# Kernel tuning notes

Hardware: AMD Instinct MI355X
Metric: run time of the kernel (lower is better)

## Reference

```python
import jax, jax.numpy as jnp
import numpy as np

EPS = 1e-10
B, S, D, K = 8, 2048, 512, 1024
TEMP = 1.0  # quantizer temperature set to 1.0 in SQVAE.__init__


def _ln(x, g, b):
    m = x.mean(-1, keepdims=True)
    v = x.var(-1, keepdims=True)
    return (x - m) / jnp.sqrt(v + 1e-5) * g + b


def _mlp(x, w1, b1, g1, be1, w2, b2, g2, be2):
    # feed_forward: Linear -> ReLU -> LayerNorm, twice (MLPLayers=2)
    h = _ln(jax.nn.relu(x @ w1 + b1), g1, be1)
    return _ln(jax.nn.relu(h @ w2 + b2), g2, be2)


def setup_inputs() -> dict:
    key = jax.random.key(0)
    ks = jax.random.split(key, 20)
    W = 0.04  # small init scale to keep distances / softmax well-conditioned
    p = lambda k, sh, s=1.0: jax.random.normal(k, sh, dtype=jnp.float32) * s
    return {
        'x': p(ks[0], (B, S, D)),
        'gumbel_u': jax.random.uniform(ks[1], (B * S, K), dtype=jnp.float32),
        'enc_w1': p(ks[2], (D, D), W), 'enc_b1': jnp.zeros(D, jnp.float32),
        'enc_g1': jnp.ones(D, jnp.float32), 'enc_be1': jnp.zeros(D, jnp.float32),
        'enc_w2': p(ks[3], (D, D), W), 'enc_b2': jnp.zeros(D, jnp.float32),
        'enc_g2': jnp.ones(D, jnp.float32), 'enc_be2': jnp.zeros(D, jnp.float32),
        'dec_w1': p(ks[4], (D, D), W), 'dec_b1': jnp.zeros(D, jnp.float32),
        'dec_g1': jnp.ones(D, jnp.float32), 'dec_be1': jnp.zeros(D, jnp.float32),
        'dec_w2': p(ks[5], (D, D), W), 'dec_b2': jnp.zeros(D, jnp.float32),
        'dec_g2': jnp.ones(D, jnp.float32), 'dec_be2': jnp.zeros(D, jnp.float32),
        'codebook': p(ks[6], (K, D)),
        'log_param_q': jnp.zeros((), jnp.float32),
    }


def reference(x, gumbel_u, enc_w1, enc_b1, enc_g1, enc_be1, enc_w2, enc_b2, enc_g2, enc_be2,
              dec_w1, dec_b1, dec_g1, dec_be1, dec_w2, dec_b2, dec_g2, dec_be2,
              codebook, log_param_q):
    bs, seq, d = x.shape
    z = _mlp(x, enc_w1, enc_b1, enc_g1, enc_be1, enc_w2, enc_b2, enc_g2, enc_be2)
    # gaussian_1: log_var_q = 0 -> var_q = exp(log_param_q_scalar)
    var_q = jnp.exp(log_param_q)
    w = 0.5 / jnp.clip(var_q, 1e-10)  # 0.5 * precision_q (scalar)
    zf = z.reshape(-1, d)  # [N, D]
    # cdist^2 style distance, scaled by weight -> logits [N, K]
    dist = w * (jnp.sum(zf * zf, axis=1, keepdims=True)
                + jnp.sum(codebook * codebook, axis=1)
                - 2.0 * zf @ codebook.T)
    logit = -dist
    logp = jax.nn.log_softmax(logit, axis=-1)
    probs = jnp.exp(logp)
    # gumbel-softmax sample (train path), noise provided as uniform input
    g = -jnp.log(-jnp.log(gumbel_u + EPS) + EPS)
    encodings = jax.nn.softmax((logit + g) / TEMP, axis=-1)
    z_q = (encodings @ codebook).reshape(bs, seq, d)
    kld_discrete = jnp.sum(probs * logp) / bs
    kld_continuous = jnp.mean(jnp.sum((z - z_q) ** 2 * w, axis=(1, 2)))
    loss = kld_discrete + kld_continuous
    avg_probs = jnp.mean(jax.lax.stop_gradient(probs), axis=0)
    perplexity = jnp.exp(-jnp.sum(avg_probs * jnp.log(avg_probs + 1e-7)))
    x_rec = _mlp(z_q, dec_w1, dec_b1, dec_g1, dec_be1, dec_w2, dec_b2, dec_g2, dec_be2)
    return x_rec, loss, perplexity
```

## Files before the change

### kernel.cpp

```cpp
#include <hip/hip_runtime.h>
#include <math.h>

#define NROWS 16384
#define DIM   512
#define KCODE 1024

typedef __attribute__((ext_vector_type(8))) __bf16 bf16x8;
typedef __attribute__((ext_vector_type(4))) float f32x4;

__device__ __forceinline__ float wave_reduce_sum(float v) {
  #pragma unroll
  for (int m = 1; m < 64; m <<= 1) v += __shfl_xor(v, m, 64);
  return v;
}
__device__ __forceinline__ float wave_reduce_max(float v) {
  #pragma unroll
  for (int m = 1; m < 64; m <<= 1) v = fmaxf(v, __shfl_xor(v, m, 64));
  return v;
}
__device__ __forceinline__ unsigned short f2bf(float f) {
  union { float f; unsigned u; } v; v.f = f;
  unsigned r = v.u + 0x7FFFu + ((v.u >> 16) & 1u);
  return (unsigned short)(r >> 16);
}
__device__ __forceinline__ float bf2f(unsigned short h) {
  union { unsigned u; float f; } v; v.u = ((unsigned)h) << 16;
  return v.f;
}
__device__ __forceinline__ uint4 pack8(const float* x) {
  uint4 r;
  r.x = (unsigned)f2bf(x[0]) | ((unsigned)f2bf(x[1]) << 16);
  r.y = (unsigned)f2bf(x[2]) | ((unsigned)f2bf(x[3]) << 16);
  r.z = (unsigned)f2bf(x[4]) | ((unsigned)f2bf(x[5]) << 16);
  r.w = (unsigned)f2bf(x[6]) | ((unsigned)f2bf(x[7]) << 16);
  return r;
}

__device__ __forceinline__ void glds16(const void* g, void* lds) {
  __builtin_amdgcn_global_load_lds(
      (const __attribute__((address_space(1))) unsigned int*)g,
      (__attribute__((address_space(3))) unsigned int*)lds, 16, 0, 0);
}

__global__ __launch_bounds__(512, 2) void dist_fused(
    const unsigned short* __restrict__ zhp, const unsigned short* __restrict__ zlp,
    const unsigned short* __restrict__ cbh, const unsigned short* __restrict__ cbl,
    const float* __restrict__ znorm, const float* __restrict__ cnorm,
    const float* __restrict__ lpq, float* __restrict__ outf) {
  __shared__ char smem[131072];
  const int t = threadIdx.x;
  const int l = t & 63, w = t >> 6;
  const int wm = w >> 2, wn = w & 3;
  const int b = blockIdx.x;
  const int xcd = b & 7, j = b >> 3;
  const int m0 = (xcd * 8 + j / 4) * 256;
  const int n0 = (j % 4) * 256;

  f32x4 acc[8][4];
  #pragma unroll
  for (int i = 0; i < 8; ++i)
    #pragma unroll
    for (int jj = 0; jj < 4; ++jj) acc[i][jj] = (f32x4){0.f, 0.f, 0.f, 0.f};

  const int row = l & 15;
  const int kcol = (l >> 4) * 8;
  const size_t aLo = (size_t)(m0 + w * 16 + row) * 512 + kcol;
  const size_t aHi = aLo + (size_t)128 * 512;
  const size_t bLo = (size_t)(n0 + w * 16 + row) * 512 + kcol;
  const size_t bHi = bLo + (size_t)128 * 512;
  const int dLo = w * 2048, dHi = (w + 8) * 2048;

  #pragma unroll 1
  for (int s = 0; s < 8; ++s) {
    const int kt = s * 64;
    #pragma unroll
    for (int js = 0; js < 2; ++js) {
      const int ko = kt + js * 32;
      const int dj = js * 1024;
      glds16(zhp + aLo + ko, smem + dLo + dj);
      glds16(zhp + aHi + ko, smem + dHi + dj);
      glds16(zlp + aLo + ko, smem + 32768 + dLo + dj);
      glds16(zlp + aHi + ko, smem + 32768 + dHi + dj);
      glds16(cbh + bLo + ko, smem + 65536 + dLo + dj);
      glds16(cbh + bHi + ko, smem + 65536 + dHi + dj);
      glds16(cbl + bLo + ko, smem + 98304 + dLo + dj);
      glds16(cbl + bHi + ko, smem + 98304 + dHi + dj);
    }
    asm volatile("s_waitcnt vmcnt(0)" ::: "memory");
    __builtin_amdgcn_s_barrier();
    #pragma unroll
    for (int js = 0; js < 2; ++js) {
      const int dj = js * 1024;
      bf16x8 af[8], bh_[4], bl_[4];
      #pragma unroll
      for (int i = 0; i < 4; ++i) {
        bh_[i] = *(const bf16x8*)(smem + 65536 + (wn * 4 + i) * 2048 + dj + l * 16);
        bl_[i] = *(const bf16x8*)(smem + 98304 + (wn * 4 + i) * 2048 + dj + l * 16);
      }
      #pragma unroll
      for (int i = 0; i < 8; ++i)
        af[i] = *(const bf16x8*)(smem + (wm * 8 + i) * 2048 + dj + l * 16);
      #pragma unroll
      for (int mi = 0; mi < 8; ++mi)
        #pragma unroll
        for (int ni = 0; ni < 4; ++ni) {
          acc[mi][ni] = __builtin_amdgcn_mfma_f32_16x16x32_bf16(af[mi], bh_[ni], acc[mi][ni], 0, 0, 0);
          acc[mi][ni] = __builtin_amdgcn_mfma_f32_16x16x32_bf16(af[mi], bl_[ni], acc[mi][ni], 0, 0, 0);
        }
      #pragma unroll
      for (int i = 0; i < 8; ++i)
        af[i] = *(const bf16x8*)(smem + 32768 + (wm * 8 + i) * 2048 + dj + l * 16);
      #pragma unroll
      for (int mi = 0; mi < 8; ++mi)
        #pragma unroll
        for (int ni = 0; ni < 4; ++ni)
          acc[mi][ni] = __builtin_amdgcn_mfma_f32_16x16x32_bf16(af[mi], bh_[ni], acc[mi][ni], 0, 0, 0);
    }
    __builtin_amdgcn_s_barrier();
  }

  float* slab = (float*)(smem + w * 4352);
  const int q = l >> 4, c16 = l & 15;
  const int c4 = (l & 15) * 4;
  const float wq = 0.5f / fmaxf(expf(lpq[0]), 1e-10f);

  #pragma unroll
  for (int mi = 0; mi < 8; ++mi) {
    __syncthreads();
    #pragma unroll
    for (int ni = 0; ni < 4; ++ni)
      #pragma unroll
      for (int r = 0; r < 4; ++r)
        slab[(q * 4 + r) * 68 + ni * 16 + c16] = acc[mi][ni][r];
    __syncthreads();
    #pragma unroll
    for (int pp = 0; pp < 4; ++pp) {
      const int rw = pp * 4 + q;
      const float4 v4 = *(const float4*)&slab[rw * 68 + c4];
      const int m = m0 + wm * 128 + mi * 16 + rw;
      const int nc = n0 + wn * 64 + c4;
      const float zn = znorm[m];
      const float4 cn = *(const float4*)&cnorm[nc];
      float4 o;
      o.x = -wq * (zn + cn.x - 2.f * v4.x);
      o.y = -wq * (zn + cn.y - 2.f * v4.y);
      o.z = -wq * (zn + cn.z - 2.f * v4.z);
      o.w = -wq * (zn + cn.w - 2.f * v4.w);
      *(float4*)&outf[(size_t)m * KCODE + nc] = o;
    }
  }
}

template <int EPI, int K, int N, int LDA>
__global__ __launch_bounds__(256) void gemm_bt(
    const unsigned short* A0, const unsigned short* B0,
    const float* __restrict__ bias, const float* __restrict__ lpq,
    const unsigned short* __restrict__ zh, const unsigned short* __restrict__ zl,
    float* __restrict__ kldc, unsigned short* __restrict__ outb) {
  __shared__ char smem[65536];
  const int t = threadIdx.x;
  const int l = t & 63, w = t >> 6;
  const int wm = w >> 1, wn = w & 1;
  const int NTN = N / 128;
  const int b = blockIdx.x;
  const int xcd = b & 7;
  const int j = b >> 3;
  const int m0 = (xcd * 16 + j / NTN) * 128;
  const int n0 = (j % NTN) * 128;

  f32x4 acc[4][4];
  #pragma unroll
  for (int i = 0; i < 4; ++i)
    #pragma unroll
    for (int jj = 0; jj < 4; ++jj) acc[i][jj] = (f32x4){0.f, 0.f, 0.f, 0.f};

  const int row = l & 15;
  const int kcol = (l >> 4) * 8;
  const size_t oA0 = (size_t)(m0 + w * 16 + row) * LDA + kcol;
  const size_t oA1 = oA0 + (size_t)64 * LDA;
  const size_t oB0 = (size_t)(n0 + w * 16 + row) * K + kcol;
  const size_t oB1 = oB0 + (size_t)64 * K;
  const int dLo = w * 2048, dHi = (w + 4) * 2048;

  constexpr int NSTEP = K / 64;

  auto issue = [&](int ss) {
    char* hb = smem + (ss & 1) * 32768;
    const int kt = ss * 64;
    #pragma unroll
    for (int js = 0; js < 2; ++js) {
      const int ko = kt + js * 32;
      const int dj = js * 1024;
      glds16(A0 + oA0 + ko, hb + dLo + dj);
      glds16(A0 + oA1 + ko, hb + dHi + dj);
      glds16(B0 + oB0 + ko, hb + 16384 + dLo + dj);
      glds16(B0 + oB1 + ko, hb + 16384 + dHi + dj);
    }
  };

  issue(0);
  #pragma unroll 1
  for (int s = 0; s < NSTEP; ++s) {
    if (s + 1 < NSTEP) {
      issue(s + 1);
      asm volatile("s_waitcnt vmcnt(8)" ::: "memory");
    } else {
      asm volatile("s_waitcnt vmcnt(0)" ::: "memory");
    }
    __builtin_amdgcn_s_barrier();
    const char* hb = smem + (s & 1) * 32768;
    #pragma unroll
    for (int js = 0; js < 2; ++js) {
      const int dj = js * 1024;
      bf16x8 af[4], bfr[4];
      #pragma unroll
      for (int i = 0; i < 4; ++i) {
        af[i]  = *(const bf16x8*)(hb + (wm * 4 + i) * 2048 + dj + l * 16);
        bfr[i] = *(const bf16x8*)(hb + 16384 + (wn * 4 + i) * 2048 + dj + l * 16);
      }
      #pragma unroll
      for (int mi = 0; mi < 4; ++mi)
        #pragma unroll
        for (int ni = 0; ni < 4; ++ni)
          acc[mi][ni] = __builtin_amdgcn_mfma_f32_16x16x32_bf16(af[mi], bfr[ni], acc[mi][ni], 0, 0, 0);
    }
    __builtin_amdgcn_s_barrier();
  }

  float* slab = (float*)(smem + w * 4352);
  const int q = l >> 4, c16 = l & 15;
  const int c4 = (l & 15) * 4;
  const float wq = (EPI == 2) ? 0.5f / fmaxf(expf(lpq[0]), 1e-10f) : 0.f;
  float local = 0.f;

  #pragma unroll
  for (int mi = 0; mi < 4; ++mi) {
    __syncthreads();
    #pragma unroll
    for (int ni = 0; ni < 4; ++ni)
      #pragma unroll
      for (int r = 0; r < 4; ++r)
        slab[(q * 4 + r) * 68 + ni * 16 + c16] = acc[mi][ni][r];
    __syncthreads();
    #pragma unroll
    for (int pp = 0; pp < 4; ++pp) {
      const int rw = pp * 4 + q;
      const float4 v4 = *(const float4*)&slab[rw * 68 + c4];
      float v[4] = {v4.x, v4.y, v4.z, v4.w};
      const int m = m0 + wm * 64 + mi * 16 + rw;
      const int nc = n0 + wn * 64 + c4;
      if (EPI == 0) {
        const float4 b4 = *(const float4*)&bias[nc];
        v[0] = fmaxf(v[0] + b4.x, 0.f);
        v[1] = fmaxf(v[1] + b4.y, 0.f);
        v[2] = fmaxf(v[2] + b4.z, 0.f);
        v[3] = fmaxf(v[3] + b4.w, 0.f);
        uint2 st;
        st.x = (unsigned)f2bf(v[0]) | ((unsigned)f2bf(v[1]) << 16);
        st.y = (unsigned)f2bf(v[2]) | ((unsigned)f2bf(v[3]) << 16);
        *(uint2*)&outb[(size_t)m * N + nc] = st;
      } else {
        const uint2 h2 = *(const uint2*)&zh[(size_t)m * N + nc];
        const uint2 l2 = *(const uint2*)&zl[(size_t)m * N + nc];
        const float z0 = bf2f((unsigned short)(h2.x & 0xFFFF)) + bf2f((unsigned short)(l2.x & 0xFFFF));
        const float z1 = bf2f((unsigned short)(h2.x >> 16))    + bf2f((unsigned short)(l2.x >> 16));
        const float z2 = bf2f((unsigned short)(h2.y & 0xFFFF)) + bf2f((unsigned short)(l2.y & 0xFFFF));
        const float z3 = bf2f((unsigned short)(h2.y >> 16))    + bf2f((unsigned short)(l2.y >> 16));
        const float d0 = z0 - v[0], d1 = z1 - v[1], d2 = z2 - v[2], d3 = z3 - v[3];
        local += d0 * d0 + d1 * d1 + d2 * d2 + d3 * d3;
        uint2 st;
        st.x = (unsigned)f2bf(v[0]) | ((unsigned)f2bf(v[1]) << 16);
        st.y = (unsigned)f2bf(v[2]) | ((unsigned)f2bf(v[3]) << 16);
        *(uint2*)&outb[(size_t)m * N + nc] = st;
      }
    }
  }
  if (EPI == 2) {
    local = wave_reduce_sum(local) * wq;
    if (l == 0) atomicAdd(kldc, local);
  }
}

template <int MODE>
__global__ __launch_bounds__(256) void ln_rows(
    const unsigned short* __restrict__ X, const float* __restrict__ g,
    const float* __restrict__ be, unsigned short* __restrict__ Y,
    unsigned short* __restrict__ Yl, float* __restrict__ znorm,
    float* __restrict__ Yf) {
  const int l = threadIdx.x & 63, wv = threadIdx.x >> 6;
  float gv[8], bv[8];
  {
    const float4 a = *(const float4*)&g[l * 8];
    const float4 b = *(const float4*)&g[l * 8 + 4];
    gv[0] = a.x; gv[1] = a.y; gv[2] = a.z; gv[3] = a.w;
    gv[4] = b.x; gv[5] = b.y; gv[6] = b.z; gv[7] = b.w;
    const float4 c = *(const float4*)&be[l * 8];
    const float4 d = *(const float4*)&be[l * 8 + 4];
    bv[0] = c.x; bv[1] = c.y; bv[2] = c.z; bv[3] = c.w;
    bv[4] = d.x; bv[5] = d.y; bv[6] = d.z; bv[7] = d.w;
  }
  const int row0 = blockIdx.x * 32 + wv * 8;
  for (int rr = 0; rr < 8; ++rr) {
    const int row = row0 + rr;
    const uint4 raw = *(const uint4*)&X[(size_t)row * 512 + l * 8];
    float v[8];
    const unsigned rw[4] = {raw.x, raw.y, raw.z, raw.w};
    #pragma unroll
    for (int i = 0; i < 4; ++i) {
      v[2 * i]     = bf2f((unsigned short)(rw[i] & 0xFFFF));
      v[2 * i + 1] = bf2f((unsigned short)(rw[i] >> 16));
    }
    float s = 0.f, ss = 0.f;
    #pragma unroll
    for (int i = 0; i < 8; ++i) { s += v[i]; ss += v[i] * v[i]; }
    #pragma unroll
    for (int m = 1; m < 64; m <<= 1) {
      s += __shfl_xor(s, m, 64);
      ss += __shfl_xor(ss, m, 64);
    }
    const float mean = s * (1.f / 512.f);
    const float var = ss * (1.f / 512.f) - mean * mean;
    const float rstd = rsqrtf(var + 1e-5f);
    float y[8];
    #pragma unroll
    for (int i = 0; i < 8; ++i) y[i] = (v[i] - mean) * rstd * gv[i] + bv[i];
    if (MODE == 0) {
      *(uint4*)&Y[(size_t)row * 512 + l * 8] = pack8(y);
    } else if (MODE == 1) {
      float lo[8], ns = 0.f;
      unsigned short hx[8];
      #pragma unroll
      for (int i = 0; i < 8; ++i) {
        hx[i] = f2bf(y[i]);
        lo[i] = y[i] - bf2f(hx[i]);
        ns += y[i] * y[i];
      }
      uint4 hv;
      hv.x = (unsigned)hx[0] | ((unsigned)hx[1] << 16);
      hv.y = (unsigned)hx[2] | ((unsigned)hx[3] << 16);
      hv.z = (unsigned)hx[4] | ((unsigned)hx[5] << 16);
      hv.w = (unsigned)hx[6] | ((unsigned)hx[7] << 16);
      *(uint4*)&Y[(size_t)row * 512 + l * 8] = hv;
      *(uint4*)&Yl[(size_t)row * 512 + l * 8] = pack8(lo);
      ns = wave_reduce_sum(ns);
      if (l == 0) znorm[row] = ns;
    } else {
      float4 o0, o1;
      o0.x = y[0]; o0.y = y[1]; o0.z = y[2]; o0.w = y[3];
      o1.x = y[4]; o1.y = y[5]; o1.z = y[6]; o1.w = y[7];
      *(float4*)&Yf[(size_t)row * 512 + l * 8] = o0;
      *(float4*)&Yf[(size_t)row * 512 + l * 8 + 4] = o1;
    }
  }
}

__global__ __launch_bounds__(256) void convert_f32_bf16(
    const float* __restrict__ X, unsigned short* __restrict__ Y) {
  const size_t i = ((size_t)blockIdx.x * 256 + threadIdx.x) * 8;
  const float4 a = *(const float4*)&X[i];
  const float4 b = *(const float4*)&X[i + 4];
  float v[8] = {a.x, a.y, a.z, a.w, b.x, b.y, b.z, b.w};
  *(uint4*)&Y[i] = pack8(v);
}

__global__ __launch_bounds__(256) void prep_cb(
    const float* __restrict__ CB, unsigned short* __restrict__ H,
    unsigned short* __restrict__ L, float* __restrict__ cnorm) {
  const int wv = threadIdx.x >> 6, l = threadIdx.x & 63;
  const int r = blockIdx.x * 4 + wv;
  const float* row = &CB[(size_t)r * 512 + l * 8];
  const float4 a = *(const float4*)row;
  const float4 b = *(const float4*)(row + 4);
  float x[8] = {a.x, a.y, a.z, a.w, b.x, b.y, b.z, b.w};
  float s = 0.f, lo[8];
  unsigned short hi[8];
  #pragma unroll
  for (int i = 0; i < 8; ++i) {
    s += x[i] * x[i];
    hi[i] = f2bf(x[i]);
    lo[i] = x[i] - bf2f(hi[i]);
  }
  uint4 hv;
  hv.x = (unsigned)hi[0] | ((unsigned)hi[1] << 16);
  hv.y = (unsigned)hi[2] | ((unsigned)hi[3] << 16);
  hv.z = (unsigned)hi[4] | ((unsigned)hi[5] << 16);
  hv.w = (unsigned)hi[6] | ((unsigned)hi[7] << 16);
  *(uint4*)&H[(size_t)r * 512 + l * 8] = hv;
  *(uint4*)&L[(size_t)r * 512 + l * 8] = pack8(lo);
  s = wave_reduce_sum(s);
  if (l == 0) cnorm[r] = s;
}

__global__ __launch_bounds__(256) void transpose_f32_bf16(
    const float* __restrict__ in, unsigned short* __restrict__ out, int R, int C) {
  __shared__ float tile[32][33];
  const int ntc = C >> 5;
  const int c0 = (blockIdx.x % ntc) * 32, r0 = (blockIdx.x / ntc) * 32;
  const int tx = threadIdx.x & 31, ty = threadIdx.x >> 5;
  #pragma unroll
  for (int i = 0; i < 4; ++i)
    tile[ty + 8 * i][tx] = in[(size_t)(r0 + ty + 8 * i) * C + c0 + tx];
  __syncthreads();
  #pragma unroll
  for (int i = 0; i < 4; ++i)
    out[(size_t)(c0 + ty + 8 * i) * R + r0 + tx] = f2bf(tile[tx][ty + 8 * i]);
}

__global__ __launch_bounds__(256) void softmax_gumbel(
    const float* logits, const float* __restrict__ U, unsigned short* E,
    float* __restrict__ colsum, float* __restrict__ kldd_acc) {
  __shared__ float cs[1024];
  __shared__ float kd[4];
  const int t = threadIdx.x;
  const int wv = t >> 6, l = t & 63;
  #pragma unroll
  for (int i = 0; i < 4; ++i) cs[t + 256 * i] = 0.f;
  __syncthreads();
  float psum[16];
  #pragma unroll
  for (int i = 0; i < 16; ++i) psum[i] = 0.f;
  float kldd = 0.f;
  const int nbase = blockIdx.x * 16 + wv * 4;

  for (int it = 0; it < 4; ++it) {
    const int row = nbase + it;
    const size_t off = (size_t)row * KCODE + 4 * l;
    float v[16];
    #pragma unroll
    for (int jj = 0; jj < 4; ++jj) {
      const float4 t4 = *(const float4*)&logits[off + 256 * jj];
      v[4 * jj + 0] = t4.x; v[4 * jj + 1] = t4.y; v[4 * jj + 2] = t4.z; v[4 * jj + 3] = t4.w;
    }
    float m = v[0];
    #pragma unroll
    for (int i = 1; i < 16; ++i) m = fmaxf(m, v[i]);
    m = wave_reduce_max(m);
    float e[16], se = 0.f;
    #pragma unroll
    for (int i = 0; i < 16; ++i) { e[i] = __expf(v[i] - m); se += e[i]; }
    se = wave_reduce_sum(se);
    const float lz = __logf(se);
    const float inv_se = 1.f / se;
    float pl = 0.f;
    #pragma unroll
    for (int i = 0; i < 16; ++i) {
      const float p = e[i] * inv_se;
      psum[i] += p;
      pl += p * (v[i] - m - lz);
    }
    kldd += pl;
    float y[16];
    #pragma unroll
    for (int jj = 0; jj < 4; ++jj) {
      const float4 t4 = *(const float4*)&U[off + 256 * jj];
      y[4 * jj + 0] = v[4 * jj + 0] - __logf(-__logf(t4.x + 1e-10f) + 1e-10f);
      y[4 * jj + 1] = v[4 * jj + 1] - __logf(-__logf(t4.y + 1e-10f) + 1e-10f);
      y[4 * jj + 2] = v[4 * jj + 2] - __logf(-__logf(t4.z + 1e-10f) + 1e-10f);
      y[4 * jj + 3] = v[4 * jj + 3] - __logf(-__logf(t4.w + 1e-10f) + 1e-10f);
    }
    float m2 = y[0];
    #pragma unroll
    for (int i = 1; i < 16; ++i) m2 = fmaxf(m2, y[i]);
    m2 = wave_reduce_max(m2);
    float ey[16], s2 = 0.f;
    #pragma unroll
    for (int i = 0; i < 16; ++i) { ey[i] = __expf(y[i] - m2); s2 += ey[i]; }
    s2 = wave_reduce_sum(s2);
    const float inv = 1.f / s2;
    #pragma unroll
    for (int jj = 0; jj < 4; ++jj) {
      ushort4 e4;
      e4.x = f2bf(ey[4 * jj + 0] * inv);
      e4.y = f2bf(ey[4 * jj + 1] * inv);
      e4.z = f2bf(ey[4 * jj + 2] * inv);
      e4.w = f2bf(ey[4 * jj + 3] * inv);
      *(ushort4*)&E[(size_t)row * 2048 + 4 * l + 256 * jj] = e4;
    }
  }
  #pragma unroll
  for (int jj = 0; jj < 4; ++jj)
    #pragma unroll
    for (int c = 0; c < 4; ++c)
      atomicAdd(&cs[256 * jj + 4 * l + c], psum[4 * jj + c]);
  kldd = wave_reduce_sum(kldd);
  if (l == 0) kd[wv] = kldd;
  __syncthreads();
  #pragma unroll
  for (int i = 0; i < 4; ++i) {
    const float vv = cs[t + 256 * i];
    if (vv != 0.f) atomicAdd(&colsum[t + 256 * i], vv);
  }
  if (t == 0) atomicAdd(kldd_acc, kd[0] + kd[1] + kd[2] + kd[3]);
}

__global__ __launch_bounds__(256) void finalize(
    const float* __restrict__ colsum, const float* __restrict__ scal,
    float* __restrict__ out) {
  const int t = threadIdx.x;
  float ent = 0.f;
  #pragma unroll
  for (int jj = 0; jj < 4; ++jj) {
    const float a = colsum[t + 256 * jj] * (1.f / 16384.f);
    ent += a * logf(a + 1e-7f);
  }
  ent = wave_reduce_sum(ent);
  __shared__ float red[4];
  if ((t & 63) == 0) red[t >> 6] = ent;
  __syncthreads();
  if (t == 0) {
    const float tot = red[0] + red[1] + red[2] + red[3];
    out[0] = (scal[0] + scal[1]) * (1.f / 8.f);
    out[1] = expf(-tot);
  }
}

extern "C" void kernel_launch(void* const* d_in, const int* in_sizes, int n_in,
                              void* d_out, int out_size, void* d_ws, size_t ws_size,
                              hipStream_t stream) {
  const float* x      = (const float*)d_in[0];
  const float* gu     = (const float*)d_in[1];
  const float* enc_w1 = (const float*)d_in[2];
  const float* enc_b1 = (const float*)d_in[3];
  const float* enc_g1 = (const float*)d_in[4];
  const float* enc_e1 = (const float*)d_in[5];
  const float* enc_w2 = (const float*)d_in[6];
  const float* enc_b2 = (const float*)d_in[7];
  const float* enc_g2 = (const float*)d_in[8];
  const float* enc_e2 = (const float*)d_in[9];
  const float* dec_w1 = (const float*)d_in[10];
  const float* dec_b1 = (const float*)d_in[11];
  const float* dec_g1 = (const float*)d_in[12];
  const float* dec_e1 = (const float*)d_in[13];
  const float* dec_w2 = (const float*)d_in[14];
  const float* dec_b2 = (const float*)d_in[15];
  const float* dec_g2 = (const float*)d_in[16];
  const float* dec_e2 = (const float*)d_in[17];
  const float* cb     = (const float*)d_in[18];
  const float* lpq    = (const float*)d_in[19];
  float* out = (float*)d_out;
  char* wsb = (char*)d_ws;

  float*          logits = (float*)(wsb + 0);
  unsigned short* Eb     = (unsigned short*)(wsb + 0);
  unsigned short* t1     = (unsigned short*)(wsb + 67108864);
  unsigned short* xb     = (unsigned short*)(wsb + 83886080);
  unsigned short* zh     = xb;
  unsigned short* hq     = (unsigned short*)(wsb + 100663296);
  unsigned short* zl     = (unsigned short*)(wsb + 117440512);
  unsigned short* wt0    = (unsigned short*)(wsb + 134217728);
  unsigned short* wt1    = wt0 + 262144;
  unsigned short* wt2    = wt1 + 262144;
  unsigned short* wt3    = wt2 + 262144;
  unsigned short* cbh    = (unsigned short*)(wsb + 136314880);
  unsigned short* cbl    = (unsigned short*)(wsb + 137363456);
  unsigned short* cbT    = (unsigned short*)(wsb + 138412032);
  float*          znorm  = (float*)(wsb + 139460608);
  float*          cnorm  = (float*)(wsb + 139526144);
  float*          colsum = (float*)(wsb + 139530240);
  float*          scal   = (float*)(wsb + 139534336);

  hipMemsetAsync(colsum, 0, 4096 + 16, stream);

  convert_f32_bf16<<<4096, 256, 0, stream>>>(x, xb);
  prep_cb<<<256, 256, 0, stream>>>(cb, cbh, cbl, cnorm);
  transpose_f32_bf16<<<256, 256, 0, stream>>>(enc_w1, wt0, 512, 512);
  transpose_f32_bf16<<<256, 256, 0, stream>>>(enc_w2, wt1, 512, 512);
  transpose_f32_bf16<<<256, 256, 0, stream>>>(dec_w1, wt2, 512, 512);
  transpose_f32_bf16<<<256, 256, 0, stream>>>(dec_w2, wt3, 512, 512);
  transpose_f32_bf16<<<512, 256, 0, stream>>>(cb, cbT, 1024, 512);

  gemm_bt<0, 512, 512, 512><<<512, 256, 0, stream>>>(
      xb, wt0, enc_b1, nullptr, nullptr, nullptr, nullptr, t1);
  ln_rows<0><<<512, 256, 0, stream>>>(t1, enc_g1, enc_e1, hq, nullptr, nullptr, nullptr);
  gemm_bt<0, 512, 512, 512><<<512, 256, 0, stream>>>(
      hq, wt1, enc_b2, nullptr, nullptr, nullptr, nullptr, t1);
  ln_rows<1><<<512, 256, 0, stream>>>(t1, enc_g2, enc_e2, zh, zl, znorm, nullptr);
  dist_fused<<<256, 512, 0, stream>>>(
      zh, zl, cbh, cbl, znorm, cnorm, lpq, logits);
  softmax_gumbel<<<1024, 256, 0, stream>>>(logits, gu, Eb, colsum, &scal[0]);
  gemm_bt<2, 1024, 512, 2048><<<512, 256, 0, stream>>>(
      Eb, cbT, nullptr, lpq, zh, zl, &scal[1], hq);
  gemm_bt<0, 512, 512, 512><<<512, 256, 0, stream>>>(
      hq, wt2, dec_b1, nullptr, nullptr, nullptr, nullptr, t1);
  ln_rows<0><<<512, 256, 0, stream>>>(t1, dec_g1, dec_e1, zl, nullptr, nullptr, nullptr);
  gemm_bt<0, 512, 512, 512><<<512, 256, 0, stream>>>(
      zl, wt3, dec_b2, nullptr, nullptr, nullptr, nullptr, t1);
  ln_rows<2><<<512, 256, 0, stream>>>(t1, dec_g2, dec_e2, nullptr, nullptr, nullptr, out);
  finalize<<<1, 256, 0, stream>>>(colsum, scal, out + 8388608);
}
```

Measured before the change: 469.9 us.

## Shrink dist_fused tiles to 128x128 and double-buffer LDS loads

```diff
diff --git a/kernel.cpp b/kernel.cpp
--- a/kernel.cpp
+++ b/kernel.cpp
@@ -42,80 +42,82 @@
       (__attribute__((address_space(3))) unsigned int*)lds, 16, 0, 0);
 }
 
-__global__ __launch_bounds__(512, 2) void dist_fused(
+__global__ __launch_bounds__(256) void dist_fused(
     const unsigned short* __restrict__ zhp, const unsigned short* __restrict__ zlp,
     const unsigned short* __restrict__ cbh, const unsigned short* __restrict__ cbl,
     const float* __restrict__ znorm, const float* __restrict__ cnorm,
     const float* __restrict__ lpq, float* __restrict__ outf) {
-  __shared__ char smem[131072];
+  __shared__ char smem[65536];
   const int t = threadIdx.x;
   const int l = t & 63, w = t >> 6;
-  const int wm = w >> 2, wn = w & 3;
+  const int wm = w >> 1, wn = w & 1;
   const int b = blockIdx.x;
   const int xcd = b & 7, j = b >> 3;
-  const int m0 = (xcd * 8 + j / 4) * 256;
-  const int n0 = (j % 4) * 256;
-
-  f32x4 acc[8][4];
-  #pragma unroll
-  for (int i = 0; i < 8; ++i)
+  const int m0 = (xcd * 16 + j / 8) * 128;
+  const int n0 = (j % 8) * 128;
+
+  f32x4 acc[4][4];
+  #pragma unroll
+  for (int i = 0; i < 4; ++i)
     #pragma unroll
     for (int jj = 0; jj < 4; ++jj) acc[i][jj] = (f32x4){0.f, 0.f, 0.f, 0.f};
 
   const int row = l & 15;
   const int kcol = (l >> 4) * 8;
   const size_t aLo = (size_t)(m0 + w * 16 + row) * 512 + kcol;
-  const size_t aHi = aLo + (size_t)128 * 512;
+  const size_t aHi = aLo + (size_t)64 * 512;
   const size_t bLo = (size_t)(n0 + w * 16 + row) * 512 + kcol;
-  const size_t bHi = bLo + (size_t)128 * 512;
-  const int dLo = w * 2048, dHi = (w + 8) * 2048;
-
+  const size_t bHi = bLo + (size_t)64 * 512;
+  const int dLo = w * 1024, dHi = (w + 4) * 1024;
+
+  auto issue = [&](int s) {
+    char* hb = smem + (s & 1) * 32768;
+    const int kt = s * 32;
+    glds16(zhp + aLo + kt, hb + dLo);
+    glds16(zhp + aHi + kt, hb + dHi);
+    glds16(zlp + aLo + kt, hb + 8192 + dLo);
+    glds16(zlp + aHi + kt, hb + 8192 + dHi);
+    glds16(cbh + bLo + kt, hb + 16384 + dLo);
+    glds16(cbh + bHi + kt, hb + 16384 + dHi);
+    glds16(cbl + bLo + kt, hb + 24576 + dLo);
+    glds16(cbl + bHi + kt, hb + 24576 + dHi);
+  };
+
+  issue(0);
   #pragma unroll 1
-  for (int s = 0; s < 8; ++s) {
-    const int kt = s * 64;
-    #pragma unroll
-    for (int js = 0; js < 2; ++js) {
-      const int ko = kt + js * 32;
-      const int dj = js * 1024;
-      glds16(zhp + aLo + ko, smem + dLo + dj);
-      glds16(zhp + aHi + ko, smem + dHi + dj);
-      glds16(zlp + aLo + ko, smem + 32768 + dLo + dj);
-      glds16(zlp + aHi + ko, smem + 32768 + dHi + dj);
-      glds16(cbh + bLo + ko, smem + 65536 + dLo + dj);
-      glds16(cbh + bHi + ko, smem + 65536 + dHi + dj);
-      glds16(cbl + bLo + ko, smem + 98304 + dLo + dj);
-      glds16(cbl + bHi + ko, smem + 98304 + dHi + dj);
-    }
-    asm volatile("s_waitcnt vmcnt(0)" ::: "memory");
+  for (int s = 0; s < 16; ++s) {
+    if (s + 1 < 16) {
+      issue(s + 1);
+      asm volatile("s_waitcnt vmcnt(8)" ::: "memory");
+    } else {
+      asm volatile("s_waitcnt vmcnt(0)" ::: "memory");
+    }
     __builtin_amdgcn_s_barrier();
-    #pragma unroll
-    for (int js = 0; js < 2; ++js) {
-      const int dj = js * 1024;
-      bf16x8 af[8], bh_[4], bl_[4];
-      #pragma unroll
-      for (int i = 0; i < 4; ++i) {
-        bh_[i] = *(const bf16x8*)(smem + 65536 + (wn * 4 + i) * 2048 + dj + l * 16);
-        bl_[i] = *(const bf16x8*)(smem + 98304 + (wn * 4 + i) * 2048 + dj + l * 16);
+    const char* hb = smem + (s & 1) * 32768;
+    bf16x8 af[4], bh_[4], bl_[4];
+    #pragma unroll
+    for (int i = 0; i < 4; ++i) {
+      bh_[i] = *(const bf16x8*)(hb + 16384 + (wn * 4 + i) * 1024 + l * 16);
+      bl_[i] = *(const bf16x8*)(hb + 24576 + (wn * 4 + i) * 1024 + l * 16);
+    }
+    #pragma unroll
+    for (int i = 0; i < 4; ++i)
+      af[i] = *(const bf16x8*)(hb + (wm * 4 + i) * 1024 + l * 16);
+    #pragma unroll
+    for (int mi = 0; mi < 4; ++mi)
+      #pragma unroll
+      for (int ni = 0; ni < 4; ++ni) {
+        acc[mi][ni] = __builtin_amdgcn_mfma_f32_16x16x32_bf16(af[mi], bh_[ni], acc[mi][ni], 0, 0, 0);
+        acc[mi][ni] = __builtin_amdgcn_mfma_f32_16x16x32_bf16(af[mi], bl_[ni], acc[mi][ni], 0, 0, 0);
       }
-      #pragma unroll
-      for (int i = 0; i < 8; ++i)
-        af[i] = *(const bf16x8*)(smem + (wm * 8 + i) * 2048 + dj + l * 16);
-      #pragma unroll
-      for (int mi = 0; mi < 8; ++mi)
-        #pragma unroll
-        for (int ni = 0; ni < 4; ++ni) {
-          acc[mi][ni] = __builtin_amdgcn_mfma_f32_16x16x32_bf16(af[mi], bh_[ni], acc[mi][ni], 0, 0, 0);
-          acc[mi][ni] = __builtin_amdgcn_mfma_f32_16x16x32_bf16(af[mi], bl_[ni], acc[mi][ni], 0, 0, 0);
-        }
-      #pragma unroll
-      for (int i = 0; i < 8; ++i)
-        af[i] = *(const bf16x8*)(smem + 32768 + (wm * 8 + i) * 2048 + dj + l * 16);
-      #pragma unroll
-      for (int mi = 0; mi < 8; ++mi)
-        #pragma unroll
-        for (int ni = 0; ni < 4; ++ni)
-          acc[mi][ni] = __builtin_amdgcn_mfma_f32_16x16x32_bf16(af[mi], bh_[ni], acc[mi][ni], 0, 0, 0);
-    }
+    #pragma unroll
+    for (int i = 0; i < 4; ++i)
+      af[i] = *(const bf16x8*)(hb + 8192 + (wm * 4 + i) * 1024 + l * 16);
+    #pragma unroll
+    for (int mi = 0; mi < 4; ++mi)
+      #pragma unroll
+      for (int ni = 0; ni < 4; ++ni)
+        acc[mi][ni] = __builtin_amdgcn_mfma_f32_16x16x32_bf16(af[mi], bh_[ni], acc[mi][ni], 0, 0, 0);
     __builtin_amdgcn_s_barrier();
   }
 
@@ -125,7 +127,7 @@
   const float wq = 0.5f / fmaxf(expf(lpq[0]), 1e-10f);
 
   #pragma unroll
-  for (int mi = 0; mi < 8; ++mi) {
+  for (int mi = 0; mi < 4; ++mi) {
     __syncthreads();
     #pragma unroll
     for (int ni = 0; ni < 4; ++ni)
@@ -137,7 +139,7 @@
     for (int pp = 0; pp < 4; ++pp) {
       const int rw = pp * 4 + q;
       const float4 v4 = *(const float4*)&slab[rw * 68 + c4];
-      const int m = m0 + wm * 128 + mi * 16 + rw;
+      const int m = m0 + wm * 64 + mi * 16 + rw;
       const int nc = n0 + wn * 64 + c4;
       const float zn = znorm[m];
       const float4 cn = *(const float4*)&cnorm[nc];
@@ -575,7 +577,7 @@
   gemm_bt<0, 512, 512, 512><<<512, 256, 0, stream>>>(
       hq, wt1, enc_b2, nullptr, nullptr, nullptr, nullptr, t1);
   ln_rows<1><<<512, 256, 0, stream>>>(t1, enc_g2, enc_e2, zh, zl, znorm, nullptr);
-  dist_fused<<<256, 512, 0, stream>>>(
+  dist_fused<<<1024, 256, 0, stream>>>(
       zh, zl, cbh, cbl, znorm, cnorm, lpq, logits);
   softmax_gumbel<<<1024, 256, 0, stream>>>(logits, gu, Eb, colsum, &scal[0]);
   gemm_bt<2, 1024, 512, 2048><<<512, 256, 0, stream>>>(
```

New measurement: 471.3 us. No clear change (+0.3%).

## Double-buffer distance GEMM K-tiles and overlap global loads with MFMA

Applied to the files above, without the earlier changes.

```diff
diff --git a/kernel.cpp b/kernel.cpp
--- a/kernel.cpp
+++ b/kernel.cpp
@@ -68,54 +68,73 @@
   const size_t aHi = aLo + (size_t)128 * 512;
   const size_t bLo = (size_t)(n0 + w * 16 + row) * 512 + kcol;
   const size_t bHi = bLo + (size_t)128 * 512;
-  const int dLo = w * 2048, dHi = (w + 8) * 2048;
-
+
+  auto issue = [&](int s) {
+    char* hb = smem + (s & 1) * 65536;
+    const int kt = s * 32;
+    glds16(zhp + aLo + kt, hb + w * 1024);
+    glds16(zhp + aHi + kt, hb + (w + 8) * 1024);
+    glds16(zlp + aLo + kt, hb + 16384 + w * 1024);
+    glds16(zlp + aHi + kt, hb + 16384 + (w + 8) * 1024);
+    glds16(cbh + bLo + kt, hb + 32768 + w * 1024);
+    glds16(cbh + bHi + kt, hb + 32768 + (w + 8) * 1024);
+    glds16(cbl + bLo + kt, hb + 49152 + w * 1024);
+    glds16(cbl + bHi + kt, hb + 49152 + (w + 8) * 1024);
+  };
+
+  issue(0);
   #pragma unroll 1
-  for (int s = 0; s < 8; ++s) {
-    const int kt = s * 64;
-    #pragma unroll
-    for (int js = 0; js < 2; ++js) {
-      const int ko = kt + js * 32;
-      const int dj = js * 1024;
-      glds16(zhp + aLo + ko, smem + dLo + dj);
-      glds16(zhp + aHi + ko, smem + dHi + dj);
-      glds16(zlp + aLo + ko, smem + 32768 + dLo + dj);
-      glds16(zlp + aHi + ko, smem + 32768 + dHi + dj);
-      glds16(cbh + bLo + ko, smem + 65536 + dLo + dj);
-      glds16(cbh + bHi + ko, smem + 65536 + dHi + dj);
-      glds16(cbl + bLo + ko, smem + 98304 + dLo + dj);
-      glds16(cbl + bHi + ko, smem + 98304 + dHi + dj);
-    }
-    asm volatile("s_waitcnt vmcnt(0)" ::: "memory");
+  for (int s = 0; s < 16; ++s) {
+    if (s + 1 < 16) {
+      issue(s + 1);
+      asm volatile("s_waitcnt vmcnt(8)" ::: "memory");
+    } else {
+      asm volatile("s_waitcnt vmcnt(0)" ::: "memory");
+    }
     __builtin_amdgcn_s_barrier();
-    #pragma unroll
-    for (int js = 0; js < 2; ++js) {
-      const int dj = js * 1024;
-      bf16x8 af[8], bh_[4], bl_[4];
-      #pragma unroll
-      for (int i = 0; i < 4; ++i) {
-        bh_[i] = *(const bf16x8*)(smem + 65536 + (wn * 4 + i) * 2048 + dj + l * 16);
-        bl_[i] = *(const bf16x8*)(smem + 98304 + (wn * 4 + i) * 2048 + dj + l * 16);
-      }
-      #pragma unroll
-      for (int i = 0; i < 8; ++i)
-        af[i] = *(const bf16x8*)(smem + (wm * 8 + i) * 2048 + dj + l * 16);
-      #pragma unroll
-      for (int mi = 0; mi < 8; ++mi)
-        #pragma unroll
-        for (int ni = 0; ni < 4; ++ni) {
-          acc[mi][ni] = __builtin_amdgcn_mfma_f32_16x16x32_bf16(af[mi], bh_[ni], acc[mi][ni], 0, 0, 0);
-          acc[mi][ni] = __builtin_amdgcn_mfma_f32_16x16x32_bf16(af[mi], bl_[ni], acc[mi][ni], 0, 0, 0);
-        }
-      #pragma unroll
-      for (int i = 0; i < 8; ++i)
-        af[i] = *(const bf16x8*)(smem + 32768 + (wm * 8 + i) * 2048 + dj + l * 16);
-      #pragma unroll
-      for (int mi = 0; mi < 8; ++mi)
-        #pragma unroll
-        for (int ni = 0; ni < 4; ++ni)
-          acc[mi][ni] = __builtin_amdgcn_mfma_f32_16x16x32_bf16(af[mi], bh_[ni], acc[mi][ni], 0, 0, 0);
-    }
+    const char* hb = smem + (s & 1) * 65536;
+    bf16x8 af[8], bh_[4], bl_[4];
+
+    #pragma unroll
+    for (int i = 0; i < 4; ++i)
+      bh_[i] = *(const bf16x8*)(hb + 32768 + (wn * 4 + i) * 1024 + l * 16);
+    #pragma unroll
+    for (int i = 0; i < 8; ++i)
+      af[i] = *(const bf16x8*)(hb + (wm * 8 + i) * 1024 + l * 16);
+    asm volatile("s_waitcnt lgkmcnt(0)" ::: "memory");
+    __builtin_amdgcn_s_setprio(1);
+    #pragma unroll
+    for (int mi = 0; mi < 8; ++mi)
+      #pragma unroll
+      for (int ni = 0; ni < 4; ++ni)
+        acc[mi][ni] = __builtin_amdgcn_mfma_f32_16x16x32_bf16(af[mi], bh_[ni], acc[mi][ni], 0, 0, 0);
+    __builtin_amdgcn_s_setprio(0);
+    __builtin_amdgcn_s_barrier();
+
+    #pragma unroll
+    for (int i = 0; i < 4; ++i)
+      bl_[i] = *(const bf16x8*)(hb + 49152 + (wn * 4 + i) * 1024 + l * 16);
+    asm volatile("s_waitcnt lgkmcnt(0)" ::: "memory");
+    __builtin_amdgcn_s_setprio(1);
+    #pragma unroll
+    for (int mi = 0; mi < 8; ++mi)
+      #pragma unroll
+      for (int ni = 0; ni < 4; ++ni)
+        acc[mi][ni] = __builtin_amdgcn_mfma_f32_16x16x32_bf16(af[mi], bl_[ni], acc[mi][ni], 0, 0, 0);
+    __builtin_amdgcn_s_setprio(0);
+    __builtin_amdgcn_s_barrier();
+
+    #pragma unroll
+    for (int i = 0; i < 8; ++i)
+      af[i] = *(const bf16x8*)(hb + 16384 + (wm * 8 + i) * 1024 + l * 16);
+    asm volatile("s_waitcnt lgkmcnt(0)" ::: "memory");
+    __builtin_amdgcn_s_setprio(1);
+    #pragma unroll
+    for (int mi = 0; mi < 8; ++mi)
+      #pragma unroll
+      for (int ni = 0; ni < 4; ++ni)
+        acc[mi][ni] = __builtin_amdgcn_mfma_f32_16x16x32_bf16(af[mi], bh_[ni], acc[mi][ni], 0, 0, 0);
+    __builtin_amdgcn_s_setprio(0);
     __builtin_amdgcn_s_barrier();
   }
 
```

New measurement: 462.3 us. About the same (-1.6%).
